# Kernel tuning notes

Measured on AMD Instinct MI355X. Metric: run time of the kernel, lower is better.

The kernel has to match this reference:

```python
import jax, jax.numpy as jnp
import numpy as np

E, B, F_IN = 24, 8192, 15
H1, H2, H3 = 512, 512, 256


def setup_inputs() -> dict:
    key = jax.random.key(0)
    ks = jax.random.split(key, 6)
    return {
        "features": jax.random.normal(ks[0], (B, F_IN), dtype=jnp.float32),
        "model_index": jax.random.randint(ks[1], (B,), 0, E, dtype=jnp.int32),
        "W1": jax.random.normal(ks[2], (E, F_IN, H1), dtype=jnp.float32) * 0.1,
        "b1": jnp.zeros((E, H1), dtype=jnp.float32),
        "W2": jax.random.normal(ks[3], (E, H1, H2), dtype=jnp.float32) * 0.05,
        "b2": jnp.zeros((E, H2), dtype=jnp.float32),
        "W3": jax.random.normal(ks[4], (E, H2, H3), dtype=jnp.float32) * 0.05,
        "b3": jnp.zeros((E, H3), dtype=jnp.float32),
        "W4": jax.random.normal(ks[5], (E, H3, 1), dtype=jnp.float32) * 0.05,
        "b4": jnp.zeros((E, 1), dtype=jnp.float32),
    }


def reference(features, model_index, W1, b1, W2, b2, W3, b3, W4, b4):
    # Run every expert MLP over the full batch (as the original does), then
    # gather the selected expert's output per sample.
    h = jax.nn.relu(jnp.einsum("bi,eih->ebh", features, W1) + b1[:, None, :])  # [E,B,H1]
    h = jax.nn.relu(jnp.einsum("ebh,ehk->ebk", h, W2) + b2[:, None, :])        # [E,B,H2]
    h = jax.nn.relu(jnp.einsum("ebk,ekm->ebm", h, W3) + b3[:, None, :])        # [E,B,H3]
    stacked = jnp.einsum("ebm,emo->ebo", h, W4) + b4[:, None, :]               # [E,B,1]
    # gather_nd equivalent: pick expert model_index[b] for each sample b
    out = stacked[model_index, jnp.arange(stacked.shape[1])]                   # [B,1]
    return out
```

## Files before the change

kernel.cpp:

```cpp
#include <hip/hip_runtime.h>

#define NE 24
#define NB 8192
#define FIN 15
#define H1 512
#define H2 512
#define H3 256
#define TS 64
#define SLOTS 130
#define GRIDM (8 * SLOTS)
#define PACKBLK 4803

#define WS_OFF 0
#define WS_XN  32
#define WS_XT  64
#define WS_ORD 4096
#define WB_BYTE 65536
#define OW1 0
#define OW2 393216
#define OW3 6684672
#define OW4 9830400

typedef __attribute__((ext_vector_type(8))) short short8v;
typedef __attribute__((ext_vector_type(4))) float f32x4;

__device__ __forceinline__ unsigned short f2bf(float x) {
  unsigned int u = __float_as_uint(x);
  unsigned int r = (u + 0x7fffu + ((u >> 16) & 1u)) >> 16;
  return (unsigned short)r;
}
__device__ __forceinline__ float bf2f(unsigned short h) {
  return __uint_as_float(((unsigned int)h) << 16);
}

__global__ __launch_bounds__(256) void k_pack(
    const float* __restrict__ W1, const float* __restrict__ W2,
    const float* __restrict__ W3, const float* __restrict__ W4,
    const int* __restrict__ midx, int* __restrict__ ws,
    unsigned short* __restrict__ wb) {
  const int t = threadIdx.x;
  if (blockIdx.x == PACKBLK) {
    __shared__ int hist[NE];
    __shared__ int off[NE + 1];
    __shared__ int cur[NE];
    __shared__ int tb[NE];
    __shared__ int xn[8];
    if (t < NE) hist[t] = 0;
    __syncthreads();
    int ev[32];
    #pragma unroll
    for (int r = 0; r < 32; ++r) {
      ev[r] = midx[r * 256 + t];
      atomicAdd(&hist[ev[r]], 1);
    }
    __syncthreads();
    if (t == 0) {
      int o = 0;
      #pragma unroll
      for (int i = 0; i < NE; ++i) { off[i] = o; cur[i] = o; o += hist[i]; }
      off[NE] = o;
    }
    if (t >= 32 && t < 40) {
      const int x = t - 32;
      int o = 0;
      for (int i = x; i < NE; i += 8) { tb[i] = o; o += (hist[i] + TS - 1) / TS; }
      xn[x] = o;
    }
    __syncthreads();
    if (t < NE + 1) ws[WS_OFF + t] = off[t];
    if (t >= 32 && t < 40) ws[WS_XN + t - 32] = xn[t - 32];
    for (int e = 0; e < NE; ++e) {
      const int nt = (hist[e] + TS - 1) / TS;
      for (int k = t; k < nt; k += 256)
        ws[WS_XT + (e & 7) * SLOTS + tb[e] + k] = (e << 16) | k;
    }
    #pragma unroll
    for (int r = 0; r < 32; ++r) {
      const int p = atomicAdd(&cur[ev[r]], 1);
      ws[WS_ORD + p] = r * 256 + t;
    }
    return;
  }
  int g = blockIdx.x * 256 + t;
  const float* src;
  unsigned short* dst;
  int Kb, N, KR;
  if (g < 49152) {
    src = W1; dst = wb + OW1; Kb = 4; N = 512; KR = 15;
  } else if (g < 49152 + 786432) {
    g -= 49152; src = W2; dst = wb + OW2; Kb = 64; N = 512; KR = 512;
  } else if (g < 49152 + 786432 + 393216) {
    g -= 49152 + 786432; src = W3; dst = wb + OW3; Kb = 64; N = 256; KR = 512;
  } else {
    g -= 49152 + 786432 + 393216; src = W4; dst = wb + OW4; Kb = 32; N = 1; KR = 256;
  }
  int e = g / (Kb * N);
  int r = g % (Kb * N);
  int kb = r / N;
  int n = r % N;
  short8v v;
  #pragma unroll
  for (int j = 0; j < 8; ++j) {
    int k = kb * 8 + j;
    float f = (k < KR) ? src[((size_t)e * KR + k) * N + n] : 0.f;
    v[j] = (short)f2bf(f);
  }
  *(short8v*)(dst + (size_t)g * 8) = v;
}

template <int NT, int KS, int MT>
__device__ __forceinline__ void layer_gemm(const unsigned short* __restrict__ aLDS,
                                           const unsigned short* __restrict__ bGlob,
                                           const float* __restrict__ bias,
                                           unsigned short* __restrict__ dLDS,
                                           int N, int ncol0, int lr, int lc) {
  f32x4 acc[MT][NT];
  #pragma unroll
  for (int mt = 0; mt < MT; ++mt)
    #pragma unroll
    for (int nt = 0; nt < NT; ++nt) acc[mt][nt] = (f32x4){0.f, 0.f, 0.f, 0.f};

  const unsigned short* bbase = bGlob + ((size_t)lc * N + ncol0 + lr) * 8;
  const size_t kstep = (size_t)4 * N * 8;

  short8v bb[4][NT];
  #pragma unroll
  for (int p = 0; p < 3; ++p) {
    if (p < KS) {
      #pragma unroll
      for (int nt = 0; nt < NT; ++nt)
        bb[p][nt] = *(const short8v*)(bbase + p * kstep + nt * 128);
    }
  }
  #pragma unroll
  for (int ks = 0; ks < KS; ++ks) {
    if (ks + 3 < KS) {
      #pragma unroll
      for (int nt = 0; nt < NT; ++nt)
        bb[(ks + 3) & 3][nt] = *(const short8v*)(bbase + (ks + 3) * kstep + nt * 128);
    }
    const unsigned short* ap = aLDS + (((ks * 4 + lc) * TS) + lr) * 8;
    short8v a[MT];
    #pragma unroll
    for (int mt = 0; mt < MT; ++mt) a[mt] = *(const short8v*)(ap + mt * 128);
    #pragma unroll
    for (int nt = 0; nt < NT; ++nt)
      #pragma unroll
      for (int mt = 0; mt < MT; ++mt)
        acc[mt][nt] = __builtin_amdgcn_mfma_f32_16x16x32_bf16(a[mt], bb[ks & 3][nt], acc[mt][nt], 0, 0, 0);
  }
  #pragma unroll
  for (int nt = 0; nt < NT; ++nt) {
    const int col = ncol0 + nt * 16 + lr;
    const float bv = bias[col];
    #pragma unroll
    for (int mt = 0; mt < MT; ++mt) {
      #pragma unroll
      for (int j = 0; j < 4; ++j) {
        const int row = mt * 16 + lc * 4 + j;
        const float v = fmaxf(acc[mt][nt][j] + bv, 0.f);
        dLDS[(((col >> 3) * TS) + row) * 8 + (col & 7)] = f2bf(v);
      }
    }
  }
}

__global__ __launch_bounds__(512, 2) void k_mlp(
    const float* __restrict__ features,
    const float* __restrict__ b1, const float* __restrict__ b2,
    const float* __restrict__ b3, const float* __restrict__ b4,
    const int* __restrict__ ws, const unsigned short* __restrict__ wb,
    float* __restrict__ out) {
  __shared__ int sidx[TS];
  __shared__ __align__(16) unsigned short fA[4][TS][8];
  __shared__ __align__(16) unsigned short actA[64][TS][8];
  __shared__ __align__(16) unsigned short actB[64][TS][8];

  const int t = threadIdx.x;
  const int wv = t >> 6;
  const int ln = t & 63;
  const int lr = ln & 15;
  const int lc = ln >> 4;

  const int bid = blockIdx.x;
  const int xcd = bid & 7;
  const int slot = bid >> 3;
  if (slot >= ws[WS_XN + xcd]) return;
  const int packed = ws[WS_XT + xcd * SLOTS + slot];
  const int e = packed >> 16;
  const int tt = packed & 0xffff;
  const int start = ws[WS_OFF + e] + tt * TS;
  const int cnt = min(TS, ws[WS_OFF + e + 1] - start);

  if (t < TS) sidx[t] = (t < cnt) ? ws[WS_ORD + start + t] : ws[WS_ORD + start];
  __syncthreads();

  if (t < 256) {
    int m = t >> 2, cb = t & 3;
    #pragma unroll
    for (int j = 0; j < 8; ++j) {
      int k = cb * 8 + j;
      fA[cb][m][j] = (k < FIN) ? f2bf(features[(size_t)sidx[m] * FIN + k]) : 0;
    }
  }
  __syncthreads();

  const unsigned short* w1p = wb + OW1 + (size_t)e * 4 * 512 * 8;
  const unsigned short* w2p = wb + OW2 + (size_t)e * 64 * 512 * 8;
  const unsigned short* w3p = wb + OW3 + (size_t)e * 64 * 256 * 8;
  const unsigned short* w4p = wb + OW4 + (size_t)e * 256;

  layer_gemm<4, 1, 4>(&fA[0][0][0], w1p, b1 + e * H1, &actA[0][0][0], 512, wv * 64, lr, lc);
  __syncthreads();
  layer_gemm<4, 16, 4>(&actA[0][0][0], w2p, b2 + e * H2, &actB[0][0][0], 512, wv * 64, lr, lc);
  __syncthreads();
  layer_gemm<2, 16, 4>(&actB[0][0][0], w3p, b3 + e * H3, &actA[0][0][0], 256, wv * 32, lr, lc);
  __syncthreads();

  {
    int m = t >> 3, c = t & 7;
    float p = 0.f;
    #pragma unroll
    for (int kk = 0; kk < 32; ++kk)
      p += bf2f(actA[0][0][(kk * TS + m) * 8 + c]) * bf2f(w4p[kk * 8 + c]);
    p += __shfl_xor(p, 1);
    p += __shfl_xor(p, 2);
    p += __shfl_xor(p, 4);
    if (c == 0 && m < cnt) out[sidx[m]] = p + b4[e];
  }
}

extern "C" void kernel_launch(void* const* d_in, const int* in_sizes, int n_in,
                              void* d_out, int out_size, void* d_ws, size_t ws_size,
                              hipStream_t stream) {
  const float* features = (const float*)d_in[0];
  const int* midx = (const int*)d_in[1];
  const float* W1 = (const float*)d_in[2];
  const float* b1 = (const float*)d_in[3];
  const float* W2 = (const float*)d_in[4];
  const float* b2 = (const float*)d_in[5];
  const float* W3 = (const float*)d_in[6];
  const float* b3 = (const float*)d_in[7];
  const float* W4 = (const float*)d_in[8];
  const float* b4 = (const float*)d_in[9];
  int* ws = (int*)d_ws;
  unsigned short* wb = (unsigned short*)((char*)d_ws + WB_BYTE);
  float* out = (float*)d_out;

  k_pack<<<PACKBLK + 1, 256, 0, stream>>>(W1, W2, W3, W4, midx, ws, wb);
  k_mlp<<<GRIDM, 512, 0, stream>>>(features, b1, b2, b3, b4, ws, wb, out);
}
```

Baseline: 130.5 us.

## Halve expert row tile and prefetch next layer's weights across layer boundaries

Cuts the per-block row tile from 64 to 32 and doubles the tile slots, which roughly doubles the number of blocks so more CUs stay busy with 24 unevenly sized experts. The B-fragment prefetch changes from a 4-deep ring to a 2-deep ping-pong held in caller registers. The last iterations of each layer now load the first weight fragments of the next layer, hiding the global-load latency at each layer boundary. Each weight byte is reused across only 32 rows instead of 64, so total weight traffic from L2 doubles. The 2-waves-per-SIMD occupancy hint is also removed from launch bounds.

```diff
diff --git a/kernel.cpp b/kernel.cpp
--- a/kernel.cpp
+++ b/kernel.cpp
@@ -6,8 +6,8 @@
 #define H1 512
 #define H2 512
 #define H3 256
-#define TS 64
-#define SLOTS 130
+#define TS 32
+#define SLOTS 260
 #define GRIDM (8 * SLOTS)
 #define PACKBLK 4803
 
@@ -108,12 +108,15 @@
   *(short8v*)(dst + (size_t)g * 8) = v;
 }
 
-template <int NT, int KS, int MT>
-__device__ __forceinline__ void layer_gemm(const unsigned short* __restrict__ aLDS,
-                                           const unsigned short* __restrict__ bGlob,
-                                           const float* __restrict__ bias,
-                                           unsigned short* __restrict__ dLDS,
-                                           int N, int ncol0, int lr, int lc) {
+template <int NT, int KS, int MT, int NNT>
+__device__ __forceinline__ void layer_gemm(
+    const unsigned short* __restrict__ aLDS,
+    const unsigned short* __restrict__ bGlob, int N, int ncol0,
+    const float* __restrict__ bias,
+    unsigned short* __restrict__ dLDS,
+    const unsigned short* __restrict__ nextB, int nextN, int nextNcol0,
+    short8v (&pb0)[4], short8v (&pb1)[4],
+    int lr, int lc) {
   f32x4 acc[MT][NT];
   #pragma unroll
   for (int mt = 0; mt < MT; ++mt)
@@ -122,32 +125,53 @@
 
   const unsigned short* bbase = bGlob + ((size_t)lc * N + ncol0 + lr) * 8;
   const size_t kstep = (size_t)4 * N * 8;
-
-  short8v bb[4][NT];
-  #pragma unroll
-  for (int p = 0; p < 3; ++p) {
-    if (p < KS) {
-      #pragma unroll
-      for (int nt = 0; nt < NT; ++nt)
-        bb[p][nt] = *(const short8v*)(bbase + p * kstep + nt * 128);
-    }
-  }
+  const unsigned short* nbase =
+      (NNT > 0) ? nextB + ((size_t)lc * nextN + nextNcol0 + lr) * 8 : nullptr;
+  const size_t nkstep = (size_t)4 * nextN * 8;
+
   #pragma unroll
   for (int ks = 0; ks < KS; ++ks) {
-    if (ks + 3 < KS) {
-      #pragma unroll
-      for (int nt = 0; nt < NT; ++nt)
-        bb[(ks + 3) & 3][nt] = *(const short8v*)(bbase + (ks + 3) * kstep + nt * 128);
-    }
     const unsigned short* ap = aLDS + (((ks * 4 + lc) * TS) + lr) * 8;
     short8v a[MT];
     #pragma unroll
     for (int mt = 0; mt < MT; ++mt) a[mt] = *(const short8v*)(ap + mt * 128);
-    #pragma unroll
-    for (int nt = 0; nt < NT; ++nt)
-      #pragma unroll
-      for (int mt = 0; mt < MT; ++mt)
-        acc[mt][nt] = __builtin_amdgcn_mfma_f32_16x16x32_bf16(a[mt], bb[ks & 3][nt], acc[mt][nt], 0, 0, 0);
+    {
+      auto& curb = (ks & 1) ? pb1 : pb0;
+      #pragma unroll
+      for (int nt = 0; nt < NT; ++nt)
+        #pragma unroll
+        for (int mt = 0; mt < MT; ++mt)
+          acc[mt][nt] = __builtin_amdgcn_mfma_f32_16x16x32_bf16(a[mt], curb[nt], acc[mt][nt], 0, 0, 0);
+    }
+    if constexpr (KS == 1) {
+      #pragma unroll
+      for (int nt = 0; nt < NNT; ++nt) {
+        pb0[nt] = *(const short8v*)(nbase + nt * 128);
+        pb1[nt] = *(const short8v*)(nbase + nkstep + nt * 128);
+      }
+    } else {
+      const int kk = ks + 2;
+      if (kk < KS) {
+        auto& nb = (kk & 1) ? pb1 : pb0;
+        #pragma unroll
+        for (int nt = 0; nt < NT; ++nt)
+          nb[nt] = *(const short8v*)(bbase + kk * kstep + nt * 128);
+      } else if (kk == KS) {
+        if (NNT > 0) {
+          auto& nb = (KS & 1) ? pb1 : pb0;
+          #pragma unroll
+          for (int nt = 0; nt < NNT; ++nt)
+            nb[nt] = *(const short8v*)(nbase + nt * 128);
+        }
+      } else {
+        if (NNT > 0) {
+          auto& nb = ((KS + 1) & 1) ? pb1 : pb0;
+          #pragma unroll
+          for (int nt = 0; nt < NNT; ++nt)
+            nb[nt] = *(const short8v*)(nbase + nkstep + nt * 128);
+        }
+      }
+    }
   }
   #pragma unroll
   for (int nt = 0; nt < NT; ++nt) {
@@ -165,7 +189,7 @@
   }
 }
 
-__global__ __launch_bounds__(512, 2) void k_mlp(
+__global__ __launch_bounds__(512) void k_mlp(
     const float* __restrict__ features,
     const float* __restrict__ b1, const float* __restrict__ b2,
     const float* __restrict__ b3, const float* __restrict__ b4,
@@ -192,32 +216,42 @@
   const int start = ws[WS_OFF + e] + tt * TS;
   const int cnt = min(TS, ws[WS_OFF + e + 1] - start);
 
-  if (t < TS) sidx[t] = (t < cnt) ? ws[WS_ORD + start + t] : ws[WS_ORD + start];
-  __syncthreads();
-
-  if (t < 256) {
-    int m = t >> 2, cb = t & 3;
-    #pragma unroll
-    for (int j = 0; j < 8; ++j) {
-      int k = cb * 8 + j;
-      fA[cb][m][j] = (k < FIN) ? f2bf(features[(size_t)sidx[m] * FIN + k]) : 0;
-    }
-  }
-  __syncthreads();
-
   const unsigned short* w1p = wb + OW1 + (size_t)e * 4 * 512 * 8;
   const unsigned short* w2p = wb + OW2 + (size_t)e * 64 * 512 * 8;
   const unsigned short* w3p = wb + OW3 + (size_t)e * 64 * 256 * 8;
   const unsigned short* w4p = wb + OW4 + (size_t)e * 256;
 
-  layer_gemm<4, 1, 4>(&fA[0][0][0], w1p, b1 + e * H1, &actA[0][0][0], 512, wv * 64, lr, lc);
-  __syncthreads();
-  layer_gemm<4, 16, 4>(&actA[0][0][0], w2p, b2 + e * H2, &actB[0][0][0], 512, wv * 64, lr, lc);
-  __syncthreads();
-  layer_gemm<2, 16, 4>(&actB[0][0][0], w3p, b3 + e * H3, &actA[0][0][0], 256, wv * 32, lr, lc);
-  __syncthreads();
-
+  short8v pb0[4], pb1[4];
   {
+    const unsigned short* nb = w1p + ((size_t)lc * 512 + wv * 64 + lr) * 8;
+    #pragma unroll
+    for (int nt = 0; nt < 4; ++nt) pb0[nt] = *(const short8v*)(nb + nt * 128);
+  }
+
+  if (t < TS) sidx[t] = (t < cnt) ? ws[WS_ORD + start + t] : ws[WS_ORD + start];
+  __syncthreads();
+
+  if (t < 128) {
+    int m = t >> 2, cb = t & 3;
+    #pragma unroll
+    for (int j = 0; j < 8; ++j) {
+      int k = cb * 8 + j;
+      fA[cb][m][j] = (k < FIN) ? f2bf(features[(size_t)sidx[m] * FIN + k]) : 0;
+    }
+  }
+  __syncthreads();
+
+  layer_gemm<4, 1, 2, 4>(&fA[0][0][0], w1p, 512, wv * 64, b1 + e * H1,
+                         &actA[0][0][0], w2p, 512, wv * 64, pb0, pb1, lr, lc);
+  __syncthreads();
+  layer_gemm<4, 16, 2, 2>(&actA[0][0][0], w2p, 512, wv * 64, b2 + e * H2,
+                          &actB[0][0][0], w3p, 256, wv * 32, pb0, pb1, lr, lc);
+  __syncthreads();
+  layer_gemm<2, 16, 2, 0>(&actB[0][0][0], w3p, 256, wv * 32, b3 + e * H3,
+                          &actA[0][0][0], nullptr, 0, 0, pb0, pb1, lr, lc);
+  __syncthreads();
+
+  if (t < 256) {
     int m = t >> 3, c = t & 7;
     float p = 0.f;
     #pragma unroll
```

New measurement: 134.8 us. 1.03x slower.
